# Optimization experiments

Hardware: AMD Instinct MI355X
Metric: run time of the kernel (lower is better)

Reference implementation:

```python
import jax, jax.numpy as jnp
import numpy as np

N, D, H_ENC, NZ, K, H_EXP, C = 32768, 1024, 512, 64, 16, 256, 10


def setup_inputs() -> dict:
    key = jax.random.key(0)
    ks = jax.random.split(key, 12)
    s = 0.02
    return {
        "X": jax.random.normal(ks[0], (N, D), dtype=jnp.float32),
        "enc_W": jax.random.normal(ks[1], (D, H_ENC), dtype=jnp.float32) * s,
        "enc_b": jnp.zeros((H_ENC,), dtype=jnp.float32),
        "z_W": jax.random.normal(ks[2], (H_ENC, NZ), dtype=jnp.float32) * s,
        "z_b": jnp.zeros((NZ,), dtype=jnp.float32),
        "mu": jax.random.normal(ks[3], (K, NZ), dtype=jnp.float32),  # cluster_layer
        "W1": jax.random.normal(ks[4], (K, NZ, H_EXP), dtype=jnp.float32) * s,
        "b1": jnp.zeros((K, H_EXP), dtype=jnp.float32),
        "W2": jax.random.normal(ks[5], (K, H_EXP, C), dtype=jnp.float32) * s,
        "b2": jnp.zeros((K, C), dtype=jnp.float32),
    }


def reference(X, enc_W, enc_b, z_W, z_b, mu, W1, b1, W2, b2):
    # AE encoder: Linear-ReLU -> z_layer
    h = jax.nn.relu(X @ enc_W + enc_b)                 # [N, H_ENC]
    z = h @ z_W + z_b                                  # [N, NZ]
    # source_distribution (Student-t, alpha=1; exponent (alpha+1)/2 = 1)
    dist = jnp.sum((z[:, None, :] - mu[None, :, :]) ** 2, axis=-1)  # [N, K]
    q = 1.0 / (1.0 + dist)
    q = q / jnp.sum(q, axis=1, keepdims=True)          # [N, K]
    # per-expert Linear-ReLU-Linear over full batch (attention=True path)
    eh = jax.nn.relu(jnp.einsum("nd,kdh->nkh", z, W1) + b1[None])  # [N, K, H_EXP]
    logits = jnp.einsum("nkh,khc->nkc", eh, W2) + b2[None]         # [N, K, C]
    # soft combine: preds[:, c] += q[:, k] * logits[:, k, c]
    preds = jnp.einsum("nk,nkc->nc", q, logits)        # [N, C]
    return preds
```

## Files before the change

### kernel.cpp

```cpp
#include <hip/hip_runtime.h>
#include <stdint.h>

#define N_ROWS 32768
#define DIM    1024
#define HENC   512
#define NZ     64
#define KE     16
#define HEXP   256
#define NC     10

typedef __attribute__((ext_vector_type(8))) __bf16 bf16x8;
typedef __attribute__((ext_vector_type(4))) float f32x4;
typedef __attribute__((ext_vector_type(8))) unsigned short u16x8;
typedef __attribute__((ext_vector_type(4))) unsigned short u16x4;

__device__ __forceinline__ unsigned short f2bf(float f) {
    __bf16 h = (__bf16)f;
    return __builtin_bit_cast(unsigned short, h);
}

__device__ __forceinline__ void gload_lds16(void* lds, const void* gsrc) {
    __builtin_amdgcn_global_load_lds(
        (const __attribute__((address_space(1))) unsigned int*)gsrc,
        (__attribute__((address_space(3))) unsigned int*)lds,
        16, 0, 0);
}

#define SWZ(col, row) ((col) ^ (((row) & 7) << 3))

__global__ void prep_weights(const float* __restrict__ enc_W,
                             const float* __restrict__ z_W,
                             const float* __restrict__ W1,
                             const float* __restrict__ W2,
                             unsigned short* __restrict__ enc_Wt,
                             unsigned short* __restrict__ z_Wt,
                             unsigned short* __restrict__ W1t,
                             unsigned short* __restrict__ W2t) {
    int i = blockIdx.x * 256 + threadIdx.x;
    if (i < 524288) {
        int n = i >> 10, k = i & 1023;
        enc_Wt[i] = f2bf(enc_W[k * HENC + n]);
    } else if (i < 557056) {
        int i2 = i - 524288;
        int n = i2 >> 9, k = i2 & 511;
        z_Wt[i2] = f2bf(z_W[k * NZ + n]);
    } else if (i < 819200) {
        int i3 = i - 557056;
        int e = i3 >> 14, rem = i3 & 16383;
        int h = rem >> 6, d = rem & 63;
        W1t[i3] = f2bf(W1[(e * NZ + d) * HEXP + h]);
    } else if (i < 884736) {
        int i4 = i - 819200;
        int e = i4 >> 12, rem = i4 & 4095;
        int c = rem >> 8, h = rem & 255;
        W2t[i4] = (c < NC) ? f2bf(W2[(e * HEXP + h) * NC + c]) : (unsigned short)0;
    }
}

__launch_bounds__(256, 2)
__global__ void gemm1(const float* __restrict__ X,
                      const unsigned short* __restrict__ Bt,
                      const float* __restrict__ enc_b,
                      unsigned short* __restrict__ hb) {
    __shared__ unsigned short As[128][64];
    __shared__ unsigned short Bs[2][256][64];
    const int t = threadIdx.x;
    const int lane = t & 63;
    const int w = t >> 6;
    const int g = lane >> 4;
    const int l15 = lane & 15;
    const int l7 = l15 & 7;
    const int wm = (w >> 1) * 64;
    const int wn = (w & 1) * 128;

    const int bid = blockIdx.x;
    const int wgid = (bid & 7) * 64 + (bid >> 3);
    const int m0 = (wgid >> 1) * 128;
    const int n0 = (wgid & 1) * 256;

    const int arow = t >> 4, acolq = t & 15;
    const float* aptr = X + (size_t)(m0 + arow) * DIM + acolq * 4;
    const int ascol = SWZ(acolq * 4, arow);
    const int brow0 = lane >> 3;
    const int bsrccol = SWZ((lane & 7) * 8, brow0);
    const unsigned short* bptr = Bt + (size_t)(n0 + brow0) * DIM + bsrccol;

    f32x4 acc[4][8];
#pragma unroll
    for (int i = 0; i < 4; ++i)
#pragma unroll
        for (int j = 0; j < 8; ++j) acc[i][j] = f32x4{0.f, 0.f, 0.f, 0.f};

    {
#pragma unroll
        for (int it = 0; it < 8; ++it) {
            const int chunk = it * 4 + w;
            gload_lds16(&Bs[0][chunk * 8][0], bptr + (size_t)chunk * 8 * DIM);
        }
        float4 a[8];
#pragma unroll
        for (int it = 0; it < 8; ++it)
            a[it] = *(const float4*)(aptr + (size_t)it * 16 * DIM);
#pragma unroll
        for (int it = 0; it < 8; ++it) {
            u16x4 p;
            p[0] = f2bf(a[it].x); p[1] = f2bf(a[it].y);
            p[2] = f2bf(a[it].z); p[3] = f2bf(a[it].w);
            *(u16x4*)&As[it * 16 + arow][ascol] = p;
        }
    }
    __syncthreads();

    float4 an[8];
    for (int step = 0; step < 16; ++step) {
        const int cur = step & 1, nxt = cur ^ 1;

        if (step < 15) {
            const int k1 = (step + 1) * 64;
#pragma unroll
            for (int it = 0; it < 8; ++it) {
                const int chunk = it * 4 + w;
                gload_lds16(&Bs[nxt][chunk * 8][0],
                            bptr + (size_t)chunk * 8 * DIM + k1);
            }
#pragma unroll
            for (int it = 0; it < 8; ++it)
                an[it] = *(const float4*)(aptr + (size_t)it * 16 * DIM + k1);
        }

#pragma unroll
        for (int kk = 0; kk < 2; ++kk) {
            const int ko = kk * 32 + g * 8;
            const int sko = SWZ(ko, l7);
            bf16x8 af[4], bfr[8];
#pragma unroll
            for (int i = 0; i < 4; ++i)
                af[i] = *(const bf16x8*)&As[wm + i * 16 + l15][sko];
#pragma unroll
            for (int j = 0; j < 8; ++j)
                bfr[j] = *(const bf16x8*)&Bs[cur][wn + j * 16 + l15][sko];
#pragma unroll
            for (int i = 0; i < 4; ++i)
#pragma unroll
                for (int j = 0; j < 8; ++j)
                    acc[i][j] = __builtin_amdgcn_mfma_f32_16x16x32_bf16(af[i], bfr[j], acc[i][j], 0, 0, 0);
        }
        __syncthreads();

        if (step < 15) {
#pragma unroll
            for (int it = 0; it < 8; ++it) {
                u16x4 p;
                p[0] = f2bf(an[it].x); p[1] = f2bf(an[it].y);
                p[2] = f2bf(an[it].z); p[3] = f2bf(an[it].w);
                *(u16x4*)&As[it * 16 + arow][ascol] = p;
            }
        }
        __syncthreads();
    }

#pragma unroll
    for (int j = 0; j < 8; ++j) {
        int col = n0 + wn + j * 16 + l15;
        float bias = enc_b[col];
#pragma unroll
        for (int i = 0; i < 4; ++i) {
            int rbase = m0 + wm + i * 16 + g * 4;
#pragma unroll
            for (int r = 0; r < 4; ++r) {
                float v = acc[i][j][r] + bias;
                v = v > 0.f ? v : 0.f;
                hb[(size_t)(rbase + r) * HENC + col] = f2bf(v);
            }
        }
    }
}

__launch_bounds__(256, 2)
__global__ void gemm2(const unsigned short* __restrict__ hb,
                      const unsigned short* __restrict__ zWt,
                      const float* __restrict__ z_b,
                      float* __restrict__ z) {
    __shared__ unsigned short As2[2][64][64];
    const int t = threadIdx.x, lane = t & 63, w = t >> 6;
    const int g = lane >> 4, l15 = lane & 15;
    const int l7 = l15 & 7;
    const int m0 = blockIdx.x * 64;
    const int brow0 = lane >> 3;
    const int bsrccol = SWZ((lane & 7) * 8, brow0);

    f32x4 acc[4];
#pragma unroll
    for (int j = 0; j < 4; ++j) acc[j] = f32x4{0.f, 0.f, 0.f, 0.f};

#pragma unroll
    for (int it = 0; it < 2; ++it) {
        const int chunk = it * 4 + w;
        gload_lds16(&As2[0][chunk * 8][0],
                    hb + (size_t)(m0 + chunk * 8 + brow0) * HENC + bsrccol);
    }
    __syncthreads();

    for (int step = 0; step < 8; ++step) {
        const int cur = step & 1, nxt = cur ^ 1;
        bf16x8 bfr[2][4];
#pragma unroll
        for (int kk = 0; kk < 2; ++kk) {
            const int kg = step * 64 + kk * 32 + g * 8;
#pragma unroll
            for (int j = 0; j < 4; ++j)
                bfr[kk][j] = *(const bf16x8*)(zWt + (size_t)(j * 16 + l15) * HENC + kg);
        }
        if (step < 7) {
            const int k1 = (step + 1) * 64;
#pragma unroll
            for (int it = 0; it < 2; ++it) {
                const int chunk = it * 4 + w;
                gload_lds16(&As2[nxt][chunk * 8][0],
                            hb + (size_t)(m0 + chunk * 8 + brow0) * HENC + k1 + bsrccol);
            }
        }
#pragma unroll
        for (int kk = 0; kk < 2; ++kk) {
            const int ko = kk * 32 + g * 8;
            bf16x8 af = *(const bf16x8*)&As2[cur][w * 16 + l15][SWZ(ko, l7)];
#pragma unroll
            for (int j = 0; j < 4; ++j)
                acc[j] = __builtin_amdgcn_mfma_f32_16x16x32_bf16(af, bfr[kk][j], acc[j], 0, 0, 0);
        }
        __syncthreads();
    }
#pragma unroll
    for (int j = 0; j < 4; ++j) {
        int col = j * 16 + l15;
        float bias = z_b[col];
#pragma unroll
        for (int r = 0; r < 4; ++r) {
            int row = m0 + w * 16 + g * 4 + r;
            z[(size_t)row * NZ + col] = acc[j][r] + bias;
        }
    }
}

__launch_bounds__(256, 2)
__global__ void expert_kernel(const float* __restrict__ z,
                              const float* __restrict__ mu,
                              const unsigned short* __restrict__ W1t,
                              const float* __restrict__ b1,
                              const unsigned short* __restrict__ W2t,
                              const float* __restrict__ b2,
                              float* __restrict__ out) {
    __shared__ __align__(16) union SU {
        struct {
            float zs[64][68];
            float mus[16][68];
            float rn[64];
            float mun[16];
        } a;
        struct {
            unsigned short w1s[2][128][64];
            unsigned short ehs[4][16][136];
        } b;
    } su;
    __shared__ float qs[64][16];

    const int t = threadIdx.x;
    const int lane = t & 63;
    const int w = t >> 6;
    const int g = lane >> 4;
    const int l15 = lane & 15;
    const int l7 = l15 & 7;
    const int r0 = blockIdx.x * 64;

    {
#pragma unroll
        for (int it = 0; it < 4; ++it) {
            int idx = it * 256 + t;
            int r = idx >> 4, c = (idx & 15) * 4;
            *(float4*)&su.a.zs[r][c] = *(const float4*)(z + (size_t)(r0 + r) * NZ + c);
        }
        int r = t >> 4, c = (t & 15) * 4;
        *(float4*)&su.a.mus[r][c] = *(const float4*)(mu + (size_t)r * NZ + c);
    }
    __syncthreads();

    if (t < 64) {
        float s = 0.f;
#pragma unroll
        for (int dq = 0; dq < 16; ++dq) {
            float4 v = *(const float4*)&su.a.zs[t][dq * 4];
            s += v.x * v.x + v.y * v.y + v.z * v.z + v.w * v.w;
        }
        su.a.rn[t] = s;
    } else if (t < 80) {
        int k = t - 64;
        float s = 0.f;
#pragma unroll
        for (int dq = 0; dq < 16; ++dq) {
            float4 v = *(const float4*)&su.a.mus[k][dq * 4];
            s += v.x * v.x + v.y * v.y + v.z * v.z + v.w * v.w;
        }
        su.a.mun[k] = s;
    }
    __syncthreads();

    bf16x8 az[2];
#pragma unroll
    for (int ks = 0; ks < 2; ++ks) {
        int row = w * 16 + l15;
        int ko = ks * 32 + g * 8;
        float4 lo = *(const float4*)&su.a.zs[row][ko];
        float4 hi = *(const float4*)&su.a.zs[row][ko + 4];
        u16x8 tmp;
        tmp[0] = f2bf(lo.x); tmp[1] = f2bf(lo.y); tmp[2] = f2bf(lo.z); tmp[3] = f2bf(lo.w);
        tmp[4] = f2bf(hi.x); tmp[5] = f2bf(hi.y); tmp[6] = f2bf(hi.z); tmp[7] = f2bf(hi.w);
        az[ks] = __builtin_bit_cast(bf16x8, tmp);
    }
    {
        bf16x8 bmu[2];
#pragma unroll
        for (int ks = 0; ks < 2; ++ks) {
            int ko = ks * 32 + g * 8;
            float4 lo = *(const float4*)&su.a.mus[l15][ko];
            float4 hi = *(const float4*)&su.a.mus[l15][ko + 4];
            u16x8 tmp;
            tmp[0] = f2bf(lo.x); tmp[1] = f2bf(lo.y); tmp[2] = f2bf(lo.z); tmp[3] = f2bf(lo.w);
            tmp[4] = f2bf(hi.x); tmp[5] = f2bf(hi.y); tmp[6] = f2bf(hi.z); tmp[7] = f2bf(hi.w);
            bmu[ks] = __builtin_bit_cast(bf16x8, tmp);
        }
        f32x4 dacc = f32x4{0.f, 0.f, 0.f, 0.f};
#pragma unroll
        for (int ks = 0; ks < 2; ++ks)
            dacc = __builtin_amdgcn_mfma_f32_16x16x32_bf16(az[ks], bmu[ks], dacc, 0, 0, 0);
#pragma unroll
        for (int r = 0; r < 4; ++r) {
            int rl = w * 16 + g * 4 + r;
            float dist = su.a.rn[rl] - 2.f * dacc[r] + su.a.mun[l15];
            qs[rl][l15] = 1.f / (1.f + dist);
        }
    }
    __syncthreads();

    if (t < 64) {
        float s = 0.f;
#pragma unroll
        for (int k = 0; k < KE; ++k) s += qs[t][k];
        float inv = 1.f / s;
#pragma unroll
        for (int k = 0; k < KE; ++k) qs[t][k] *= inv;
    }
    __syncthreads();

    const int srow = lane >> 3;
    const int scol = SWZ((lane & 7) * 8, srow);

#pragma unroll
    for (int it = 0; it < 4; ++it) {
        const int chunk = it * 4 + w;
        gload_lds16(&su.b.w1s[0][chunk * 8][0],
                    W1t + (size_t)(chunk * 8 + srow) * NZ + scol);
    }
    __syncthreads();

    float pacc[4] = {0.f, 0.f, 0.f, 0.f};
    unsigned short* eh = &su.b.ehs[w][0][0];

    for (int e = 0; e < KE; ++e) {
        const unsigned short* w2e = W2t + e * (16 * HEXP);
        bf16x8 w2f[8];
#pragma unroll
        for (int hh = 0; hh < 8; ++hh)
            w2f[hh] = *(const bf16x8*)(w2e + (size_t)l15 * HEXP + hh * 32 + g * 8);
        float b1v[2][8];
#pragma unroll
        for (int half = 0; half < 2; ++half)
#pragma unroll
            for (int j = 0; j < 8; ++j)
                b1v[half][j] = b1[e * HEXP + half * 128 + j * 16 + l15];

        f32x4 la = f32x4{0.f, 0.f, 0.f, 0.f};
#pragma unroll
        for (int half = 0; half < 2; ++half) {
            const int i = e * 2 + half;
            const int cur = i & 1, nxt = cur ^ 1;

            if (i + 1 < 2 * KE) {
                const int eg = (i + 1) >> 1;
                const int h1 = ((i + 1) & 1) * 128;
                const unsigned short* src =
                    W1t + (size_t)eg * (HEXP * NZ) + (size_t)(h1 + srow) * NZ + scol;
#pragma unroll
                for (int it = 0; it < 4; ++it) {
                    const int chunk = it * 4 + w;
                    gload_lds16(&su.b.w1s[nxt][chunk * 8][0],
                                src + (size_t)chunk * 8 * NZ);
                }
            }

            f32x4 ea[8];
#pragma unroll
            for (int j = 0; j < 8; ++j) ea[j] = f32x4{0.f, 0.f, 0.f, 0.f};
#pragma unroll
            for (int ks = 0; ks < 2; ++ks) {
                const int sko = SWZ(ks * 32 + g * 8, l7);
#pragma unroll
                for (int j = 0; j < 8; ++j) {
                    bf16x8 bw = *(const bf16x8*)&su.b.w1s[cur][j * 16 + l15][sko];
                    ea[j] = __builtin_amdgcn_mfma_f32_16x16x32_bf16(az[ks], bw, ea[j], 0, 0, 0);
                }
            }
#pragma unroll
            for (int j = 0; j < 8; ++j) {
#pragma unroll
                for (int r = 0; r < 4; ++r) {
                    float v = ea[j][r] + b1v[half][j];
                    v = v > 0.f ? v : 0.f;
                    eh[(g * 4 + r) * 136 + j * 16 + l15] = f2bf(v);
                }
            }
#pragma unroll
            for (int ks2 = 0; ks2 < 4; ++ks2) {
                bf16x8 ef = *(const bf16x8*)&eh[l15 * 136 + ks2 * 32 + g * 8];
                la = __builtin_amdgcn_mfma_f32_16x16x32_bf16(ef, w2f[half * 4 + ks2], la, 0, 0, 0);
            }
            __syncthreads();
        }

        float b2v = (l15 < NC) ? b2[e * NC + l15] : 0.f;
#pragma unroll
        for (int r = 0; r < 4; ++r) {
            int rl = w * 16 + g * 4 + r;
            pacc[r] += qs[rl][e] * (la[r] + b2v);
        }
    }

    if (l15 < NC) {
#pragma unroll
        for (int r = 0; r < 4; ++r) {
            int row = r0 + w * 16 + g * 4 + r;
            out[(size_t)row * NC + l15] = pacc[r];
        }
    }
}

extern "C" void kernel_launch(void* const* d_in, const int* in_sizes, int n_in,
                              void* d_out, int out_size, void* d_ws, size_t ws_size,
                              hipStream_t stream) {
    const float* X     = (const float*)d_in[0];
    const float* enc_W = (const float*)d_in[1];
    const float* enc_b = (const float*)d_in[2];
    const float* z_W   = (const float*)d_in[3];
    const float* z_b   = (const float*)d_in[4];
    const float* mu    = (const float*)d_in[5];
    const float* W1    = (const float*)d_in[6];
    const float* b1    = (const float*)d_in[7];
    const float* W2    = (const float*)d_in[8];
    const float* b2    = (const float*)d_in[9];
    float* out = (float*)d_out;

    char* ws = (char*)d_ws;
    unsigned short* hb     = (unsigned short*)(ws);
    float*          z      = (float*)(ws + 33554432);
    unsigned short* enc_Wt = (unsigned short*)(ws + 41943040);
    unsigned short* z_Wt   = (unsigned short*)(ws + 42991616);
    unsigned short* W1t    = (unsigned short*)(ws + 43057152);
    unsigned short* W2t    = (unsigned short*)(ws + 43581440);

    prep_weights<<<dim3(3456), dim3(256), 0, stream>>>(enc_W, z_W, W1, W2,
                                                       enc_Wt, z_Wt, W1t, W2t);
    gemm1<<<dim3(512), dim3(256), 0, stream>>>(X, enc_Wt, enc_b, hb);
    gemm2<<<dim3(512), dim3(256), 0, stream>>>(hb, z_Wt, z_b, z);
    expert_kernel<<<dim3(512), dim3(256), 0, stream>>>(z, mu, W1t, b1, W2t, b2, out);
}
```

Baseline: 135.8 us.

## Fuse z-layer GEMM into encoder GEMM epilogue with split-K partial outputs

The encoder GEMM now keeps its ReLU'd bf16 hidden tile in shared memory, reusing the operand buffers, and immediately multiplies it by the matching half of z_W. Each of the two column-half blocks writes a partial z into its own buffer, and the expert kernel sums the two partials plus bias when loading z. This removes the separate gemm2 launch and the round trip of the 32 MB bf16 hidden activation through global memory. In exchange gemm1 gains a longer epilogue with extra syncs and register use, and z traffic doubles to two fp32 partial buffers.

```diff
diff --git a/kernel.cpp b/kernel.cpp
--- a/kernel.cpp
+++ b/kernel.cpp
@@ -61,9 +61,15 @@
 __global__ void gemm1(const float* __restrict__ X,
                       const unsigned short* __restrict__ Bt,
                       const float* __restrict__ enc_b,
-                      unsigned short* __restrict__ hb) {
-    __shared__ unsigned short As[128][64];
-    __shared__ unsigned short Bs[2][256][64];
+                      const unsigned short* __restrict__ zWt,
+                      float* __restrict__ zpart) {
+    __shared__ union G1U {
+        struct {
+            unsigned short As[128][64];
+            unsigned short Bs[2][256][64];
+        } s;
+        unsigned short hbs[128][256];
+    } u;
     const int t = threadIdx.x;
     const int lane = t & 63;
     const int w = t >> 6;
@@ -95,7 +101,7 @@
 #pragma unroll
         for (int it = 0; it < 8; ++it) {
             const int chunk = it * 4 + w;
-            gload_lds16(&Bs[0][chunk * 8][0], bptr + (size_t)chunk * 8 * DIM);
+            gload_lds16(&u.s.Bs[0][chunk * 8][0], bptr + (size_t)chunk * 8 * DIM);
         }
         float4 a[8];
 #pragma unroll
@@ -106,7 +112,7 @@
             u16x4 p;
             p[0] = f2bf(a[it].x); p[1] = f2bf(a[it].y);
             p[2] = f2bf(a[it].z); p[3] = f2bf(a[it].w);
-            *(u16x4*)&As[it * 16 + arow][ascol] = p;
+            *(u16x4*)&u.s.As[it * 16 + arow][ascol] = p;
         }
     }
     __syncthreads();
@@ -120,7 +126,7 @@
 #pragma unroll
             for (int it = 0; it < 8; ++it) {
                 const int chunk = it * 4 + w;
-                gload_lds16(&Bs[nxt][chunk * 8][0],
+                gload_lds16(&u.s.Bs[nxt][chunk * 8][0],
                             bptr + (size_t)chunk * 8 * DIM + k1);
             }
 #pragma unroll
@@ -135,10 +141,10 @@
             bf16x8 af[4], bfr[8];
 #pragma unroll
             for (int i = 0; i < 4; ++i)
-                af[i] = *(const bf16x8*)&As[wm + i * 16 + l15][sko];
+                af[i] = *(const bf16x8*)&u.s.As[wm + i * 16 + l15][sko];
 #pragma unroll
             for (int j = 0; j < 8; ++j)
-                bfr[j] = *(const bf16x8*)&Bs[cur][wn + j * 16 + l15][sko];
+                bfr[j] = *(const bf16x8*)&u.s.Bs[cur][wn + j * 16 + l15][sko];
 #pragma unroll
             for (int i = 0; i < 4; ++i)
 #pragma unroll
@@ -153,7 +159,7 @@
                 u16x4 p;
                 p[0] = f2bf(an[it].x); p[1] = f2bf(an[it].y);
                 p[2] = f2bf(an[it].z); p[3] = f2bf(an[it].w);
-                *(u16x4*)&As[it * 16 + arow][ascol] = p;
+                *(u16x4*)&u.s.As[it * 16 + arow][ascol] = p;
             }
         }
         __syncthreads();
@@ -161,89 +167,63 @@
 
 #pragma unroll
     for (int j = 0; j < 8; ++j) {
-        int col = n0 + wn + j * 16 + l15;
-        float bias = enc_b[col];
+        const int col = wn + j * 16 + l15;
+        const float bias = enc_b[n0 + col];
 #pragma unroll
         for (int i = 0; i < 4; ++i) {
-            int rbase = m0 + wm + i * 16 + g * 4;
+            const int rb = wm + i * 16 + g * 4;
 #pragma unroll
             for (int r = 0; r < 4; ++r) {
                 float v = acc[i][j][r] + bias;
                 v = v > 0.f ? v : 0.f;
-                hb[(size_t)(rbase + r) * HENC + col] = f2bf(v);
-            }
-        }
+                u.hbs[rb + r][SWZ(col, rb + r)] = f2bf(v);
+            }
+        }
+    }
+    __syncthreads();
+
+    {
+        f32x4 zacc[2][4];
+#pragma unroll
+        for (int i2 = 0; i2 < 2; ++i2)
+#pragma unroll
+            for (int j2 = 0; j2 < 4; ++j2) zacc[i2][j2] = f32x4{0.f, 0.f, 0.f, 0.f};
+
+        const unsigned short* zwB = zWt + n0;
+#pragma unroll
+        for (int ks = 0; ks < 8; ++ks) {
+            const int k = ks * 32 + g * 8;
+            bf16x8 bz[4];
+#pragma unroll
+            for (int j2 = 0; j2 < 4; ++j2)
+                bz[j2] = *(const bf16x8*)(zwB + (size_t)(j2 * 16 + l15) * HENC + k);
+#pragma unroll
+            for (int i2 = 0; i2 < 2; ++i2) {
+                const int row = w * 32 + i2 * 16 + l15;
+                bf16x8 af = *(const bf16x8*)&u.hbs[row][SWZ(k, row)];
+#pragma unroll
+                for (int j2 = 0; j2 < 4; ++j2)
+                    zacc[i2][j2] = __builtin_amdgcn_mfma_f32_16x16x32_bf16(af, bz[j2], zacc[i2][j2], 0, 0, 0);
+            }
+        }
+        float* zp = zpart + (size_t)(n0 ? 1 : 0) * N_ROWS * NZ;
+#pragma unroll
+        for (int i2 = 0; i2 < 2; ++i2)
+#pragma unroll
+            for (int j2 = 0; j2 < 4; ++j2) {
+                const int colz = j2 * 16 + l15;
+#pragma unroll
+                for (int r = 0; r < 4; ++r) {
+                    const int rowz = m0 + w * 32 + i2 * 16 + g * 4 + r;
+                    zp[(size_t)rowz * NZ + colz] = zacc[i2][j2][r];
+                }
+            }
     }
 }
 
 __launch_bounds__(256, 2)
-__global__ void gemm2(const unsigned short* __restrict__ hb,
-                      const unsigned short* __restrict__ zWt,
-                      const float* __restrict__ z_b,
-                      float* __restrict__ z) {
-    __shared__ unsigned short As2[2][64][64];
-    const int t = threadIdx.x, lane = t & 63, w = t >> 6;
-    const int g = lane >> 4, l15 = lane & 15;
-    const int l7 = l15 & 7;
-    const int m0 = blockIdx.x * 64;
-    const int brow0 = lane >> 3;
-    const int bsrccol = SWZ((lane & 7) * 8, brow0);
-
-    f32x4 acc[4];
-#pragma unroll
-    for (int j = 0; j < 4; ++j) acc[j] = f32x4{0.f, 0.f, 0.f, 0.f};
-
-#pragma unroll
-    for (int it = 0; it < 2; ++it) {
-        const int chunk = it * 4 + w;
-        gload_lds16(&As2[0][chunk * 8][0],
-                    hb + (size_t)(m0 + chunk * 8 + brow0) * HENC + bsrccol);
-    }
-    __syncthreads();
-
-    for (int step = 0; step < 8; ++step) {
-        const int cur = step & 1, nxt = cur ^ 1;
-        bf16x8 bfr[2][4];
-#pragma unroll
-        for (int kk = 0; kk < 2; ++kk) {
-            const int kg = step * 64 + kk * 32 + g * 8;
-#pragma unroll
-            for (int j = 0; j < 4; ++j)
-                bfr[kk][j] = *(const bf16x8*)(zWt + (size_t)(j * 16 + l15) * HENC + kg);
-        }
-        if (step < 7) {
-            const int k1 = (step + 1) * 64;
-#pragma unroll
-            for (int it = 0; it < 2; ++it) {
-                const int chunk = it * 4 + w;
-                gload_lds16(&As2[nxt][chunk * 8][0],
-                            hb + (size_t)(m0 + chunk * 8 + brow0) * HENC + k1 + bsrccol);
-            }
-        }
-#pragma unroll
-        for (int kk = 0; kk < 2; ++kk) {
-            const int ko = kk * 32 + g * 8;
-            bf16x8 af = *(const bf16x8*)&As2[cur][w * 16 + l15][SWZ(ko, l7)];
-#pragma unroll
-            for (int j = 0; j < 4; ++j)
-                acc[j] = __builtin_amdgcn_mfma_f32_16x16x32_bf16(af, bfr[kk][j], acc[j], 0, 0, 0);
-        }
-        __syncthreads();
-    }
-#pragma unroll
-    for (int j = 0; j < 4; ++j) {
-        int col = j * 16 + l15;
-        float bias = z_b[col];
-#pragma unroll
-        for (int r = 0; r < 4; ++r) {
-            int row = m0 + w * 16 + g * 4 + r;
-            z[(size_t)row * NZ + col] = acc[j][r] + bias;
-        }
-    }
-}
-
-__launch_bounds__(256, 2)
-__global__ void expert_kernel(const float* __restrict__ z,
+__global__ void expert_kernel(const float* __restrict__ zpart,
+                              const float* __restrict__ z_b,
                               const float* __restrict__ mu,
                               const unsigned short* __restrict__ W1t,
                               const float* __restrict__ b1,
@@ -273,11 +253,19 @@
     const int r0 = blockIdx.x * 64;
 
     {
+        const float* zp0 = zpart;
+        const float* zp1 = zpart + (size_t)N_ROWS * NZ;
 #pragma unroll
         for (int it = 0; it < 4; ++it) {
             int idx = it * 256 + t;
             int r = idx >> 4, c = (idx & 15) * 4;
-            *(float4*)&su.a.zs[r][c] = *(const float4*)(z + (size_t)(r0 + r) * NZ + c);
+            float4 a = *(const float4*)(zp0 + (size_t)(r0 + r) * NZ + c);
+            float4 b = *(const float4*)(zp1 + (size_t)(r0 + r) * NZ + c);
+            float4 zb = *(const float4*)(z_b + c);
+            float4 s;
+            s.x = a.x + b.x + zb.x; s.y = a.y + b.y + zb.y;
+            s.z = a.z + b.z + zb.z; s.w = a.w + b.w + zb.w;
+            *(float4*)&su.a.zs[r][c] = s;
         }
         int r = t >> 4, c = (t & 15) * 4;
         *(float4*)&su.a.mus[r][c] = *(const float4*)(mu + (size_t)r * NZ + c);
@@ -459,16 +447,14 @@
     float* out = (float*)d_out;
 
     char* ws = (char*)d_ws;
-    unsigned short* hb     = (unsigned short*)(ws);
-    float*          z      = (float*)(ws + 33554432);
-    unsigned short* enc_Wt = (unsigned short*)(ws + 41943040);
-    unsigned short* z_Wt   = (unsigned short*)(ws + 42991616);
-    unsigned short* W1t    = (unsigned short*)(ws + 43057152);
-    unsigned short* W2t    = (unsigned short*)(ws + 43581440);
+    float*          zpart  = (float*)(ws);
+    unsigned short* enc_Wt = (unsigned short*)(ws + 16777216);
+    unsigned short* z_Wt   = (unsigned short*)(ws + 17825792);
+    unsigned short* W1t    = (unsigned short*)(ws + 17891328);
+    unsigned short* W2t    = (unsigned short*)(ws + 18415616);
 
     prep_weights<<<dim3(3456), dim3(256), 0, stream>>>(enc_W, z_W, W1, W2,
                                                        enc_Wt, z_Wt, W1t, W2t);
-    gemm1<<<dim3(512), dim3(256), 0, stream>>>(X, enc_Wt, enc_b, hb);
-    gemm2<<<dim3(512), dim3(256), 0, stream>>>(hb, z_Wt, z_b, z);
-    expert_kernel<<<dim3(512), dim3(256), 0, stream>>>(z, mu, W1t, b1, W2t, b2, out);
-}
+    gemm1<<<dim3(512), dim3(256), 0, stream>>>(X, enc_Wt, enc_b, z_Wt, zpart);
+    expert_kernel<<<dim3(512), dim3(256), 0, stream>>>(zpart, z_b, mu, W1t, b1, W2t, b2, out);
+}
```

Result: faster. 122.5 us (-9.8%).
